# Kernel optimization log

Measured on AMD Instinct MI355X. Metric: run time of the kernel, lower is better.

Reference implementation:

```python
import math
import jax, jax.numpy as jnp
import numpy as np

B, L, D, H = 4, 512, 256, 8
DH = D // H
BUCKETS = 11  # rel_pos_buckets; padding_idx = BUCKETS


def setup_inputs() -> dict:
    key = jax.random.key(0)
    ks = jax.random.split(key, 12)
    s = 0.02
    rel_table = jax.random.normal(ks[10], (BUCKETS + 1, D), dtype=jnp.float32) * s
    rel_table = rel_table.at[BUCKETS].set(0.0)  # padding_idx row is zero
    return {
        "inputs": jax.random.normal(ks[0], (B, L, D), dtype=jnp.float32),
        "mask": jax.random.randint(ks[1], (B, L, L), 0, 2) > 0,
        "distances": jax.random.randint(ks[2], (B, L, L), 0, BUCKETS + 1),
        "Wq": jax.random.normal(ks[3], (D, D), dtype=jnp.float32) * s,
        "bq": jnp.zeros((D,), jnp.float32),
        "Wk": jax.random.normal(ks[4], (D, D), dtype=jnp.float32) * s,
        "bk": jnp.zeros((D,), jnp.float32),
        "Wv": jax.random.normal(ks[5], (D, D), dtype=jnp.float32) * s,
        "bv": jnp.zeros((D,), jnp.float32),
        "Wo": jax.random.normal(ks[6], (D, D), dtype=jnp.float32) * s,
        "bo": jnp.zeros((D,), jnp.float32),
        "rel_table": rel_table,
        "u": jax.random.normal(ks[7], (D,), dtype=jnp.float32) * s,
        "v": jax.random.normal(ks[8], (D,), dtype=jnp.float32) * s,
    }


def reference(inputs, mask, distances, Wq, bq, Wk, bk, Wv, bv, Wo, bo, rel_table, u, v):
    def shape(x):  # (B, L, D) -> (B, H, L, DH)
        return x.reshape(B, L, H, DH).transpose(0, 2, 1, 3)

    q = shape(inputs @ Wq + bq) / math.sqrt(DH)
    k = shape(inputs @ Wk + bk)
    val = shape(inputs @ Wv + bv)

    # content term: (q + u) k^T
    a_c = jnp.einsum("bhqd,bhkd->bhqk", q + u.reshape(1, H, 1, DH), k)

    # relative-position term: embedding gather (padding row already zero, mask anyway)
    valid = (distances != BUCKETS)[..., None].astype(rel_table.dtype)
    rel = (rel_table[distances] * valid).reshape(B, L, L, H, DH)  # (B, Lq, Lk, H, DH)
    b_d = jnp.einsum("bhqd,bqkhd->bhqk", q + v.reshape(1, H, 1, DH), rel)

    scores = jnp.where(mask[:, None, :, :], jnp.float32(-1e18), a_c + b_d)
    attn = jax.nn.softmax(scores, axis=-1)  # (B, H, Lq, Lk)

    ctx = jnp.einsum("bhqk,bhkd->bhqd", attn, val)
    ctx = ctx.transpose(0, 2, 1, 3).reshape(B, L, D)
    output = ctx @ Wo + bo
    return output, attn
```

## Files before the change

kernel.cpp:

```cpp
#include <hip/hip_runtime.h>
#include <math.h>

#define BB 4
#define LL 512
#define DD 256
#define HH 8
#define DHH 32
#define NB 12

__global__ __launch_bounds__(256) void qkv_kernel(const float* __restrict__ x,
    const float* __restrict__ Wq, const float* __restrict__ bq,
    const float* __restrict__ Wk, const float* __restrict__ bk,
    const float* __restrict__ Wv, const float* __restrict__ bv,
    const float* __restrict__ uvec, const float* __restrict__ vvec,
    float* __restrict__ Qu, float* __restrict__ Qv,
    float* __restrict__ KT, float* __restrict__ V) {
    __shared__ float xs[8][DD];
    const int mat = blockIdx.x >> 8;
    const int r0 = (blockIdx.x & 255) * 8;
    const int t = threadIdx.x;
    const int cg = t & 63, rg = t >> 6;
    const int c0 = cg * 4;
    {
        const float4* xg = (const float4*)(x + r0 * DD);
        float4* xsv = (float4*)&xs[0][0];
        xsv[t] = xg[t];
        xsv[t + 256] = xg[t + 256];
    }
    __syncthreads();
    const float* W    = (mat == 0) ? Wq : (mat == 1) ? Wk : Wv;
    const float* bias = (mat == 0) ? bq : (mat == 1) ? bk : bv;
    float acc[2][4];
#pragma unroll
    for (int r = 0; r < 2; ++r)
#pragma unroll
        for (int c = 0; c < 4; ++c) acc[r][c] = bias[c0 + c];
    for (int i0 = 0; i0 < DD; i0 += 4) {
        float4 wv4[4], xv4[2];
#pragma unroll
        for (int j = 0; j < 4; ++j) wv4[j] = *(const float4*)&W[(i0 + j) * DD + c0];
#pragma unroll
        for (int r = 0; r < 2; ++r) xv4[r] = *(const float4*)&xs[rg * 2 + r][i0];
        const float* wf = (const float*)wv4;
        const float* xf = (const float*)xv4;
#pragma unroll
        for (int r = 0; r < 2; ++r)
#pragma unroll
            for (int j = 0; j < 4; ++j)
#pragma unroll
                for (int c = 0; c < 4; ++c)
                    acc[r][c] = fmaf(xf[r * 4 + j], wf[j * 4 + c], acc[r][c]);
    }
    if (mat == 0) {
        const float s = 0.17677669529663687f;
        const float4 u4 = *(const float4*)&uvec[c0];
        const float4 v4 = *(const float4*)&vvec[c0];
#pragma unroll
        for (int r = 0; r < 2; ++r) {
            const int row = r0 + rg * 2 + r;
            float4 q = make_float4(acc[r][0] * s, acc[r][1] * s, acc[r][2] * s, acc[r][3] * s);
            *(float4*)&Qu[row * DD + c0] = make_float4(q.x + u4.x, q.y + u4.y, q.z + u4.z, q.w + u4.w);
            *(float4*)&Qv[row * DD + c0] = make_float4(q.x + v4.x, q.y + v4.y, q.z + v4.z, q.w + v4.w);
        }
    } else if (mat == 1) {
        const int b = r0 >> 9;
        const int kb = (r0 & 511) + rg * 2;
#pragma unroll
        for (int c = 0; c < 4; ++c) {
            const int col = c0 + c;
            const int h = col >> 5, dd = col & 31;
            float* p = KT + ((long)((b * HH + h) * DHH + dd)) * LL + kb;
            p[0] = acc[0][c];
            p[1] = acc[1][c];
        }
    } else {
#pragma unroll
        for (int r = 0; r < 2; ++r)
            *(float4*)&V[(r0 + rg * 2 + r) * DD + c0] =
                make_float4(acc[r][0], acc[r][1], acc[r][2], acc[r][3]);
    }
}

__global__ __launch_bounds__(512, 4) void scores_ctx_kernel(const float* __restrict__ Qu,
    const float* __restrict__ Qv, const float* __restrict__ KT,
    const float* __restrict__ rel_table, const int* __restrict__ mask,
    const int* __restrict__ dist, const float* __restrict__ V,
    float* __restrict__ attn, float* __restrict__ ctx) {
    __shared__ float Qs[16][DHH];
    __shared__ float Ps[16][NB];
    __shared__ float ss[16 * 512];
    const int blk = blockIdx.x;
    const int h = blk & 7;
    const int rest = blk >> 3;
    const int qt16 = rest & 31;
    const int b = rest >> 5;
    const int q0 = qt16 * 16;
    const int t = threadIdx.x;
    const int w = t >> 6, l = t & 63;

    float* Qv8  = ss;
    float* rels = ss + 512;

    {
        const int r = t >> 5, c = t & 31;
        Qs[r][c]          = Qu[(b * LL + q0 + r) * DD + h * DHH + c];
        Qv8[r * DHH + c]  = Qv[(b * LL + q0 + r) * DD + h * DHH + c];
    }
    if (t < NB * DHH) {
        rels[(t >> 5) * 33 + (t & 31)] = rel_table[(t >> 5) * DD + h * DHH + (t & 31)];
    }
    __syncthreads();
    if (t < 16 * NB) {
        const int bk = t >> 4, r = t & 15;
        float a = 0.f;
#pragma unroll
        for (int d = 0; d < DHH; ++d) a = fmaf(Qv8[r * DHH + d], rels[bk * 33 + d], a);
        Ps[r][bk] = a;
    }
    __syncthreads();

    const int r0 = 2 * w;
    const long kbase = (long)(b * HH + h) * DHH * LL;
    float e0[2][4], e1[2][4];
    float sum0 = 0.f, sum1 = 0.f;
#pragma unroll
    for (int s = 0; s < 2; ++s) {
        const int k0 = 4 * l + 256 * s;
        const int4 dx0 = *(const int4*)&dist[(b * LL + q0 + r0) * LL + k0];
        const int4 dx1 = *(const int4*)&dist[(b * LL + q0 + r0 + 1) * LL + k0];
        const int4 mx0 = *(const int4*)&mask[(b * LL + q0 + r0) * LL + k0];
        const int4 mx1 = *(const int4*)&mask[(b * LL + q0 + r0 + 1) * LL + k0];
        float s0[4], s1[4];
        s0[0] = Ps[r0][dx0.x]; s0[1] = Ps[r0][dx0.y]; s0[2] = Ps[r0][dx0.z]; s0[3] = Ps[r0][dx0.w];
        s1[0] = Ps[r0 + 1][dx1.x]; s1[1] = Ps[r0 + 1][dx1.y]; s1[2] = Ps[r0 + 1][dx1.z]; s1[3] = Ps[r0 + 1][dx1.w];
#pragma unroll
        for (int d8 = 0; d8 < DHH; d8 += 8) {
            float4 kv[8];
#pragma unroll
            for (int j = 0; j < 8; ++j)
                kv[j] = *(const float4*)&KT[kbase + (long)(d8 + j) * LL + k0];
            const float4 q0a = *(const float4*)&Qs[r0][d8];
            const float4 q0b = *(const float4*)&Qs[r0][d8 + 4];
            const float4 q1a = *(const float4*)&Qs[r0 + 1][d8];
            const float4 q1b = *(const float4*)&Qs[r0 + 1][d8 + 4];
            const float* qa0 = (const float*)&q0a;
            const float* qb0 = (const float*)&q0b;
            const float* qa1 = (const float*)&q1a;
            const float* qb1 = (const float*)&q1b;
#pragma unroll
            for (int j = 0; j < 4; ++j) {
                s0[0] = fmaf(qa0[j], kv[j].x, s0[0]);
                s0[1] = fmaf(qa0[j], kv[j].y, s0[1]);
                s0[2] = fmaf(qa0[j], kv[j].z, s0[2]);
                s0[3] = fmaf(qa0[j], kv[j].w, s0[3]);
                s1[0] = fmaf(qa1[j], kv[j].x, s1[0]);
                s1[1] = fmaf(qa1[j], kv[j].y, s1[1]);
                s1[2] = fmaf(qa1[j], kv[j].z, s1[2]);
                s1[3] = fmaf(qa1[j], kv[j].w, s1[3]);
            }
#pragma unroll
            for (int j = 0; j < 4; ++j) {
                s0[0] = fmaf(qb0[j], kv[j + 4].x, s0[0]);
                s0[1] = fmaf(qb0[j], kv[j + 4].y, s0[1]);
                s0[2] = fmaf(qb0[j], kv[j + 4].z, s0[2]);
                s0[3] = fmaf(qb0[j], kv[j + 4].w, s0[3]);
                s1[0] = fmaf(qb1[j], kv[j + 4].x, s1[0]);
                s1[1] = fmaf(qb1[j], kv[j + 4].y, s1[1]);
                s1[2] = fmaf(qb1[j], kv[j + 4].z, s1[2]);
                s1[3] = fmaf(qb1[j], kv[j + 4].w, s1[3]);
            }
        }
        e0[s][0] = mx0.x ? 0.f : __expf(s0[0]);
        e0[s][1] = mx0.y ? 0.f : __expf(s0[1]);
        e0[s][2] = mx0.z ? 0.f : __expf(s0[2]);
        e0[s][3] = mx0.w ? 0.f : __expf(s0[3]);
        e1[s][0] = mx1.x ? 0.f : __expf(s1[0]);
        e1[s][1] = mx1.y ? 0.f : __expf(s1[1]);
        e1[s][2] = mx1.z ? 0.f : __expf(s1[2]);
        e1[s][3] = mx1.w ? 0.f : __expf(s1[3]);
        sum0 += (e0[s][0] + e0[s][1]) + (e0[s][2] + e0[s][3]);
        sum1 += (e1[s][0] + e1[s][1]) + (e1[s][2] + e1[s][3]);
    }
    for (int off = 32; off > 0; off >>= 1) {
        sum0 += __shfl_xor(sum0, off);
        sum1 += __shfl_xor(sum1, off);
    }
    const float inv0 = 1.0f / sum0, inv1 = 1.0f / sum1;
    float* a0 = attn + ((long)(b * HH + h) * LL + q0 + r0) * LL;
    float* a1 = a0 + LL;
#pragma unroll
    for (int s = 0; s < 2; ++s) {
        const int k0 = 4 * l + 256 * s;
        const int ch = k0 >> 7;
        const int oct = (k0 & 127) >> 3;
        const int h4 = k0 & 4;
        const float4 o0 = make_float4(e0[s][0] * inv0, e0[s][1] * inv0, e0[s][2] * inv0, e0[s][3] * inv0);
        const float4 o1 = make_float4(e1[s][0] * inv1, e1[s][1] * inv1, e1[s][2] * inv1, e1[s][3] * inv1);
        *(float4*)&a0[k0] = o0;
        *(float4*)&a1[k0] = o1;
        *(float4*)&ss[r0 * 512 + ch * 128 + (((oct ^ (r0 >> 2)) << 3) | h4)] = o0;
        *(float4*)&ss[(r0 + 1) * 512 + ch * 128 + (((oct ^ ((r0 + 1) >> 2)) << 3) | h4)] = o1;
    }

    const int qt = t & 3;
    const int dt = (t >> 2) & 7;
    const int kg = t >> 5;
    const float* vbase = V + (long)b * LL * DD + h * DHH + dt * 4;
    float acc[4][4];
#pragma unroll
    for (int i = 0; i < 4; ++i)
#pragma unroll
        for (int jd = 0; jd < 4; ++jd) acc[i][jd] = 0.f;
    __syncthreads();
#pragma unroll 1
    for (int c = 0; c < 4; ++c) {
#pragma unroll
        for (int ki = 0; ki < 2; ++ki) {
            float4 sv[4];
#pragma unroll
            for (int i = 0; i < 4; ++i)
                sv[i] = *(const float4*)&ss[(qt * 4 + i) * 512 + c * 128 + (((kg ^ qt) << 3) | (ki << 2))];
#pragma unroll
            for (int j = 0; j < 4; ++j) {
                const int k = c * 128 + (kg << 3) + (ki << 2) + j;
                const float4 vf = *(const float4*)&vbase[k * DD];
                const float w0 = ((const float*)&sv[0])[j];
                const float w1 = ((const float*)&sv[1])[j];
                const float w2 = ((const float*)&sv[2])[j];
                const float w3 = ((const float*)&sv[3])[j];
                acc[0][0] = fmaf(w0, vf.x, acc[0][0]); acc[0][1] = fmaf(w0, vf.y, acc[0][1]);
                acc[0][2] = fmaf(w0, vf.z, acc[0][2]); acc[0][3] = fmaf(w0, vf.w, acc[0][3]);
                acc[1][0] = fmaf(w1, vf.x, acc[1][0]); acc[1][1] = fmaf(w1, vf.y, acc[1][1]);
                acc[1][2] = fmaf(w1, vf.z, acc[1][2]); acc[1][3] = fmaf(w1, vf.w, acc[1][3]);
                acc[2][0] = fmaf(w2, vf.x, acc[2][0]); acc[2][1] = fmaf(w2, vf.y, acc[2][1]);
                acc[2][2] = fmaf(w2, vf.z, acc[2][2]); acc[2][3] = fmaf(w2, vf.w, acc[2][3]);
                acc[3][0] = fmaf(w3, vf.x, acc[3][0]); acc[3][1] = fmaf(w3, vf.y, acc[3][1]);
                acc[3][2] = fmaf(w3, vf.z, acc[3][2]); acc[3][3] = fmaf(w3, vf.w, acc[3][3]);
            }
        }
    }
    __syncthreads();
#pragma unroll
    for (int i = 0; i < 4; ++i)
        *(float4*)&ss[kg * 512 + (qt * 4 + i) * 32 + dt * 4] =
            make_float4(acc[i][0], acc[i][1], acc[i][2], acc[i][3]);
    __syncthreads();
    {
        const int qr = t >> 5, dr = t & 31;
        float r = 0.f;
#pragma unroll
        for (int kg2 = 0; kg2 < 16; ++kg2) r += ss[kg2 * 512 + qr * 32 + dr];
        ctx[(b * LL + q0 + qr) * DD + h * DHH + dr] = r;
    }
}

__global__ __launch_bounds__(256) void outproj_kernel(const float* __restrict__ ctx,
    const float* __restrict__ Wo, const float* __restrict__ bo,
    float* __restrict__ out) {
    __shared__ float xs[4][DD];
    const int r0 = blockIdx.x * 4;
    const int t = threadIdx.x;
    const int rg = t >> 6;
    const int c0 = (t & 63) * 4;
    ((float4*)&xs[0][0])[t] = ((const float4*)(ctx + r0 * DD))[t];
    __syncthreads();
    float4 acc = *(const float4*)&bo[c0];
    for (int i0 = 0; i0 < DD; i0 += 8) {
        float4 wv[8];
#pragma unroll
        for (int j = 0; j < 8; ++j) wv[j] = *(const float4*)&Wo[(i0 + j) * DD + c0];
        const float4 x0 = *(const float4*)&xs[rg][i0];
        const float4 x1 = *(const float4*)&xs[rg][i0 + 4];
        const float* xf0 = (const float*)&x0;
        const float* xf1 = (const float*)&x1;
#pragma unroll
        for (int j = 0; j < 4; ++j) {
            acc.x = fmaf(xf0[j], wv[j].x, acc.x);
            acc.y = fmaf(xf0[j], wv[j].y, acc.y);
            acc.z = fmaf(xf0[j], wv[j].z, acc.z);
            acc.w = fmaf(xf0[j], wv[j].w, acc.w);
        }
#pragma unroll
        for (int j = 0; j < 4; ++j) {
            acc.x = fmaf(xf1[j], wv[j + 4].x, acc.x);
            acc.y = fmaf(xf1[j], wv[j + 4].y, acc.y);
            acc.z = fmaf(xf1[j], wv[j + 4].z, acc.z);
            acc.w = fmaf(xf1[j], wv[j + 4].w, acc.w);
        }
    }
    *(float4*)&out[(r0 + rg) * DD + c0] = acc;
}

extern "C" void kernel_launch(void* const* d_in, const int* in_sizes, int n_in,
                              void* d_out, int out_size, void* d_ws, size_t ws_size,
                              hipStream_t stream) {
    const float* x    = (const float*)d_in[0];
    const int* mk     = (const int*)d_in[1];
    const int* dist   = (const int*)d_in[2];
    const float* Wq = (const float*)d_in[3];
    const float* bq = (const float*)d_in[4];
    const float* Wk = (const float*)d_in[5];
    const float* bk = (const float*)d_in[6];
    const float* Wv = (const float*)d_in[7];
    const float* bv = (const float*)d_in[8];
    const float* Wo = (const float*)d_in[9];
    const float* bo = (const float*)d_in[10];
    const float* rel_table = (const float*)d_in[11];
    const float* uvec = (const float*)d_in[12];
    const float* vvec = (const float*)d_in[13];

    float* out  = (float*)d_out;
    float* attn = out + BB * LL * DD;

    float* Qu = (float*)d_ws;
    float* Qv = Qu + BB * LL * DD;
    float* KT = Qv + BB * LL * DD;
    float* V  = KT + BB * LL * DD;
    float* C  = V + BB * LL * DD;

    qkv_kernel<<<3 * 256, 256, 0, stream>>>(x, Wq, bq, Wk, bk, Wv, bv, uvec, vvec,
                                            Qu, Qv, KT, V);
    scores_ctx_kernel<<<BB * (LL / 16) * HH, 512, 0, stream>>>(Qu, Qv, KT, rel_table,
                                                               mk, dist, V, attn, C);
    outproj_kernel<<<BB * LL / 4, 256, 0, stream>>>(C, Wo, bo, out);
}
```

Measured before the change: 167.7 us.

## Enlarge row tiles in projection GEMMs and split score work across key halves

```diff
diff --git a/kernel.cpp b/kernel.cpp
--- a/kernel.cpp
+++ b/kernel.cpp
@@ -8,75 +8,77 @@
 #define DHH 32
 #define NB 12
 
-__global__ __launch_bounds__(256) void qkv_kernel(const float* __restrict__ x,
+__global__ __launch_bounds__(256, 4) void qkv_kernel(const float* __restrict__ x,
     const float* __restrict__ Wq, const float* __restrict__ bq,
     const float* __restrict__ Wk, const float* __restrict__ bk,
     const float* __restrict__ Wv, const float* __restrict__ bv,
     const float* __restrict__ uvec, const float* __restrict__ vvec,
     float* __restrict__ Qu, float* __restrict__ Qv,
     float* __restrict__ KT, float* __restrict__ V) {
-    __shared__ float xs[8][DD];
-    const int mat = blockIdx.x >> 8;
-    const int r0 = (blockIdx.x & 255) * 8;
+    __shared__ float xs[32][DD];
+    const int mat = blockIdx.x >> 6;
+    const int r0 = (blockIdx.x & 63) * 32;
     const int t = threadIdx.x;
     const int cg = t & 63, rg = t >> 6;
     const int c0 = cg * 4;
     {
         const float4* xg = (const float4*)(x + r0 * DD);
         float4* xsv = (float4*)&xs[0][0];
-        xsv[t] = xg[t];
-        xsv[t + 256] = xg[t + 256];
+#pragma unroll
+        for (int j = 0; j < 8; ++j) xsv[t + 256 * j] = xg[t + 256 * j];
     }
     __syncthreads();
     const float* W    = (mat == 0) ? Wq : (mat == 1) ? Wk : Wv;
     const float* bias = (mat == 0) ? bq : (mat == 1) ? bk : bv;
-    float acc[2][4];
-#pragma unroll
-    for (int r = 0; r < 2; ++r)
+    float acc[8][4];
+#pragma unroll
+    for (int r = 0; r < 8; ++r)
 #pragma unroll
         for (int c = 0; c < 4; ++c) acc[r][c] = bias[c0 + c];
     for (int i0 = 0; i0 < DD; i0 += 4) {
-        float4 wv4[4], xv4[2];
+        float4 wv4[4];
 #pragma unroll
         for (int j = 0; j < 4; ++j) wv4[j] = *(const float4*)&W[(i0 + j) * DD + c0];
-#pragma unroll
-        for (int r = 0; r < 2; ++r) xv4[r] = *(const float4*)&xs[rg * 2 + r][i0];
+        float4 xv[8];
+#pragma unroll
+        for (int r = 0; r < 8; ++r) xv[r] = *(const float4*)&xs[rg * 8 + r][i0];
         const float* wf = (const float*)wv4;
-        const float* xf = (const float*)xv4;
-#pragma unroll
-        for (int r = 0; r < 2; ++r)
+#pragma unroll
+        for (int r = 0; r < 8; ++r) {
+            const float* xf = (const float*)&xv[r];
 #pragma unroll
             for (int j = 0; j < 4; ++j)
 #pragma unroll
                 for (int c = 0; c < 4; ++c)
-                    acc[r][c] = fmaf(xf[r * 4 + j], wf[j * 4 + c], acc[r][c]);
+                    acc[r][c] = fmaf(xf[j], wf[j * 4 + c], acc[r][c]);
+        }
     }
     if (mat == 0) {
         const float s = 0.17677669529663687f;
         const float4 u4 = *(const float4*)&uvec[c0];
         const float4 v4 = *(const float4*)&vvec[c0];
 #pragma unroll
-        for (int r = 0; r < 2; ++r) {
-            const int row = r0 + rg * 2 + r;
+        for (int r = 0; r < 8; ++r) {
+            const int row = r0 + rg * 8 + r;
             float4 q = make_float4(acc[r][0] * s, acc[r][1] * s, acc[r][2] * s, acc[r][3] * s);
             *(float4*)&Qu[row * DD + c0] = make_float4(q.x + u4.x, q.y + u4.y, q.z + u4.z, q.w + u4.w);
             *(float4*)&Qv[row * DD + c0] = make_float4(q.x + v4.x, q.y + v4.y, q.z + v4.z, q.w + v4.w);
         }
     } else if (mat == 1) {
         const int b = r0 >> 9;
-        const int kb = (r0 & 511) + rg * 2;
+        const int kb = (r0 & 511) + rg * 8;
 #pragma unroll
         for (int c = 0; c < 4; ++c) {
             const int col = c0 + c;
             const int h = col >> 5, dd = col & 31;
             float* p = KT + ((long)((b * HH + h) * DHH + dd)) * LL + kb;
-            p[0] = acc[0][c];
-            p[1] = acc[1][c];
+            *(float4*)&p[0] = make_float4(acc[0][c], acc[1][c], acc[2][c], acc[3][c]);
+            *(float4*)&p[4] = make_float4(acc[4][c], acc[5][c], acc[6][c], acc[7][c]);
         }
     } else {
 #pragma unroll
-        for (int r = 0; r < 2; ++r)
-            *(float4*)&V[(r0 + rg * 2 + r) * DD + c0] =
+        for (int r = 0; r < 8; ++r)
+            *(float4*)&V[(r0 + rg * 8 + r) * DD + c0] =
                 make_float4(acc[r][0], acc[r][1], acc[r][2], acc[r][3]);
     }
 }
@@ -88,6 +90,7 @@
     float* __restrict__ attn, float* __restrict__ ctx) {
     __shared__ float Qs[16][DHH];
     __shared__ float Ps[16][NB];
+    __shared__ float psum[2][16];
     __shared__ float ss[16 * 512];
     const int blk = blockIdx.x;
     const int h = blk & 7;
@@ -119,87 +122,116 @@
     }
     __syncthreads();
 
-    const int r0 = 2 * w;
+    const int rw = w & 3, sw = w >> 2;
+    const int r0 = 4 * rw;
+    const int k0 = 4 * l + 256 * sw;
     const long kbase = (long)(b * HH + h) * DHH * LL;
-    float e0[2][4], e1[2][4];
-    float sum0 = 0.f, sum1 = 0.f;
-#pragma unroll
-    for (int s = 0; s < 2; ++s) {
-        const int k0 = 4 * l + 256 * s;
+    float s0[4], s1[4], s2[4], s3[4];
+    {
         const int4 dx0 = *(const int4*)&dist[(b * LL + q0 + r0) * LL + k0];
         const int4 dx1 = *(const int4*)&dist[(b * LL + q0 + r0 + 1) * LL + k0];
+        const int4 dx2 = *(const int4*)&dist[(b * LL + q0 + r0 + 2) * LL + k0];
+        const int4 dx3 = *(const int4*)&dist[(b * LL + q0 + r0 + 3) * LL + k0];
+        s0[0] = Ps[r0][dx0.x];     s0[1] = Ps[r0][dx0.y];     s0[2] = Ps[r0][dx0.z];     s0[3] = Ps[r0][dx0.w];
+        s1[0] = Ps[r0 + 1][dx1.x]; s1[1] = Ps[r0 + 1][dx1.y]; s1[2] = Ps[r0 + 1][dx1.z]; s1[3] = Ps[r0 + 1][dx1.w];
+        s2[0] = Ps[r0 + 2][dx2.x]; s2[1] = Ps[r0 + 2][dx2.y]; s2[2] = Ps[r0 + 2][dx2.z]; s2[3] = Ps[r0 + 2][dx2.w];
+        s3[0] = Ps[r0 + 3][dx3.x]; s3[1] = Ps[r0 + 3][dx3.y]; s3[2] = Ps[r0 + 3][dx3.z]; s3[3] = Ps[r0 + 3][dx3.w];
+    }
+#pragma unroll
+    for (int d8 = 0; d8 < DHH; d8 += 8) {
+        float4 kv[8];
+#pragma unroll
+        for (int j = 0; j < 8; ++j)
+            kv[j] = *(const float4*)&KT[kbase + (long)(d8 + j) * LL + k0];
+        const float4 q0a = *(const float4*)&Qs[r0][d8];
+        const float4 q0b = *(const float4*)&Qs[r0][d8 + 4];
+        const float4 q1a = *(const float4*)&Qs[r0 + 1][d8];
+        const float4 q1b = *(const float4*)&Qs[r0 + 1][d8 + 4];
+        const float4 q2a = *(const float4*)&Qs[r0 + 2][d8];
+        const float4 q2b = *(const float4*)&Qs[r0 + 2][d8 + 4];
+        const float4 q3a = *(const float4*)&Qs[r0 + 3][d8];
+        const float4 q3b = *(const float4*)&Qs[r0 + 3][d8 + 4];
+        const float* qa0 = (const float*)&q0a; const float* qb0 = (const float*)&q0b;
+        const float* qa1 = (const float*)&q1a; const float* qb1 = (const float*)&q1b;
+        const float* qa2 = (const float*)&q2a; const float* qb2 = (const float*)&q2b;
+        const float* qa3 = (const float*)&q3a; const float* qb3 = (const float*)&q3b;
+#pragma unroll
+        for (int j = 0; j < 4; ++j) {
+            s0[0] = fmaf(qa0[j], kv[j].x, s0[0]); s0[1] = fmaf(qa0[j], kv[j].y, s0[1]);
+            s0[2] = fmaf(qa0[j], kv[j].z, s0[2]); s0[3] = fmaf(qa0[j], kv[j].w, s0[3]);
+            s1[0] = fmaf(qa1[j], kv[j].x, s1[0]); s1[1] = fmaf(qa1[j], kv[j].y, s1[1]);
+            s1[2] = fmaf(qa1[j], kv[j].z, s1[2]); s1[3] = fmaf(qa1[j], kv[j].w, s1[3]);
+            s2[0] = fmaf(qa2[j], kv[j].x, s2[0]); s2[1] = fmaf(qa2[j], kv[j].y, s2[1]);
+            s2[2] = fmaf(qa2[j], kv[j].z, s2[2]); s2[3] = fmaf(qa2[j], kv[j].w, s2[3]);
+            s3[0] = fmaf(qa3[j], kv[j].x, s3[0]); s3[1] = fmaf(qa3[j], kv[j].y, s3[1]);
+            s3[2] = fmaf(qa3[j], kv[j].z, s3[2]); s3[3] = fmaf(qa3[j], kv[j].w, s3[3]);
+        }
+#pragma unroll
+        for (int j = 0; j < 4; ++j) {
+            s0[0] = fmaf(qb0[j], kv[j + 4].x, s0[0]); s0[1] = fmaf(qb0[j], kv[j + 4].y, s0[1]);
+            s0[2] = fmaf(qb0[j], kv[j + 4].z, s0[2]); s0[3] = fmaf(qb0[j], kv[j + 4].w, s0[3]);
+            s1[0] = fmaf(qb1[j], kv[j + 4].x, s1[0]); s1[1] = fmaf(qb1[j], kv[j + 4].y, s1[1]);
+            s1[2] = fmaf(qb1[j], kv[j + 4].z, s1[2]); s1[3] = fmaf(qb1[j], kv[j + 4].w, s1[3]);
+            s2[0] = fmaf(qb2[j], kv[j + 4].x, s2[0]); s2[1] = fmaf(qb2[j], kv[j + 4].y, s2[1]);
+            s2[2] = fmaf(qb2[j], kv[j + 4].z, s2[2]); s2[3] = fmaf(qb2[j], kv[j + 4].w, s2[3]);
+            s3[0] = fmaf(qb3[j], kv[j + 4].x, s3[0]); s3[1] = fmaf(qb3[j], kv[j + 4].y, s3[1]);
+            s3[2] = fmaf(qb3[j], kv[j + 4].z, s3[2]); s3[3] = fmaf(qb3[j], kv[j + 4].w, s3[3]);
+        }
+    }
+    float e0[4], e1[4], e2[4], e3[4];
+    {
         const int4 mx0 = *(const int4*)&mask[(b * LL + q0 + r0) * LL + k0];
         const int4 mx1 = *(const int4*)&mask[(b * LL + q0 + r0 + 1) * LL + k0];
-        float s0[4], s1[4];
-        s0[0] = Ps[r0][dx0.x]; s0[1] = Ps[r0][dx0.y]; s0[2] = Ps[r0][dx0.z]; s0[3] = Ps[r0][dx0.w];
-        s1[0] = Ps[r0 + 1][dx1.x]; s1[1] = Ps[r0 + 1][dx1.y]; s1[2] = Ps[r0 + 1][dx1.z]; s1[3] = Ps[r0 + 1][dx1.w];
-#pragma unroll
-        for (int d8 = 0; d8 < DHH; d8 += 8) {
-            float4 kv[8];
-#pragma unroll
-            for (int j = 0; j < 8; ++j)
-                kv[j] = *(const float4*)&KT[kbase + (long)(d8 + j) * LL + k0];
-            const float4 q0a = *(const float4*)&Qs[r0][d8];
-            const float4 q0b = *(const float4*)&Qs[r0][d8 + 4];
-            const float4 q1a = *(const float4*)&Qs[r0 + 1][d8];
-            const float4 q1b = *(const float4*)&Qs[r0 + 1][d8 + 4];
-            const float* qa0 = (const float*)&q0a;
-            const float* qb0 = (const float*)&q0b;
-            const float* qa1 = (const float*)&q1a;
-            const float* qb1 = (const float*)&q1b;
-#pragma unroll
-            for (int j = 0; j < 4; ++j) {
-                s0[0] = fmaf(qa0[j], kv[j].x, s0[0]);
-                s0[1] = fmaf(qa0[j], kv[j].y, s0[1]);
-                s0[2] = fmaf(qa0[j], kv[j].z, s0[2]);
-                s0[3] = fmaf(qa0[j], kv[j].w, s0[3]);
-                s1[0] = fmaf(qa1[j], kv[j].x, s1[0]);
-                s1[1] = fmaf(qa1[j], kv[j].y, s1[1]);
-                s1[2] = fmaf(qa1[j], kv[j].z, s1[2]);
-                s1[3] = fmaf(qa1[j], kv[j].w, s1[3]);
-            }
-#pragma unroll
-            for (int j = 0; j < 4; ++j) {
-                s0[0] = fmaf(qb0[j], kv[j + 4].x, s0[0]);
-                s0[1] = fmaf(qb0[j], kv[j + 4].y, s0[1]);
-                s0[2] = fmaf(qb0[j], kv[j + 4].z, s0[2]);
-                s0[3] = fmaf(qb0[j], kv[j + 4].w, s0[3]);
-                s1[0] = fmaf(qb1[j], kv[j + 4].x, s1[0]);
-                s1[1] = fmaf(qb1[j], kv[j + 4].y, s1[1]);
-                s1[2] = fmaf(qb1[j], kv[j + 4].z, s1[2]);
-                s1[3] = fmaf(qb1[j], kv[j + 4].w, s1[3]);
-            }
-        }
-        e0[s][0] = mx0.x ? 0.f : __expf(s0[0]);
-        e0[s][1] = mx0.y ? 0.f : __expf(s0[1]);
-        e0[s][2] = mx0.z ? 0.f : __expf(s0[2]);
-        e0[s][3] = mx0.w ? 0.f : __expf(s0[3]);
-        e1[s][0] = mx1.x ? 0.f : __expf(s1[0]);
-        e1[s][1] = mx1.y ? 0.f : __expf(s1[1]);
-        e1[s][2] = mx1.z ? 0.f : __expf(s1[2]);
-        e1[s][3] = mx1.w ? 0.f : __expf(s1[3]);
-        sum0 += (e0[s][0] + e0[s][1]) + (e0[s][2] + e0[s][3]);
-        sum1 += (e1[s][0] + e1[s][1]) + (e1[s][2] + e1[s][3]);
-    }
+        const int4 mx2 = *(const int4*)&mask[(b * LL + q0 + r0 + 2) * LL + k0];
+        const int4 mx3 = *(const int4*)&mask[(b * LL + q0 + r0 + 3) * LL + k0];
+        e0[0] = mx0.x ? 0.f : __expf(s0[0]); e0[1] = mx0.y ? 0.f : __expf(s0[1]);
+        e0[2] = mx0.z ? 0.f : __expf(s0[2]); e0[3] = mx0.w ? 0.f : __expf(s0[3]);
+        e1[0] = mx1.x ? 0.f : __expf(s1[0]); e1[1] = mx1.y ? 0.f : __expf(s1[1]);
+        e1[2] = mx1.z ? 0.f : __expf(s1[2]); e1[3] = mx1.w ? 0.f : __expf(s1[3]);
+        e2[0] = mx2.x ? 0.f : __expf(s2[0]); e2[1] = mx2.y ? 0.f : __expf(s2[1]);
+        e2[2] = mx2.z ? 0.f : __expf(s2[2]); e2[3] = mx2.w ? 0.f : __expf(s2[3]);
+        e3[0] = mx3.x ? 0.f : __expf(s3[0]); e3[1] = mx3.y ? 0.f : __expf(s3[1]);
+        e3[2] = mx3.z ? 0.f : __expf(s3[2]); e3[3] = mx3.w ? 0.f : __expf(s3[3]);
+    }
+    float sm0 = (e0[0] + e0[1]) + (e0[2] + e0[3]);
+    float sm1 = (e1[0] + e1[1]) + (e1[2] + e1[3]);
+    float sm2 = (e2[0] + e2[1]) + (e2[2] + e2[3]);
+    float sm3 = (e3[0] + e3[1]) + (e3[2] + e3[3]);
     for (int off = 32; off > 0; off >>= 1) {
-        sum0 += __shfl_xor(sum0, off);
-        sum1 += __shfl_xor(sum1, off);
-    }
-    const float inv0 = 1.0f / sum0, inv1 = 1.0f / sum1;
-    float* a0 = attn + ((long)(b * HH + h) * LL + q0 + r0) * LL;
-    float* a1 = a0 + LL;
-#pragma unroll
-    for (int s = 0; s < 2; ++s) {
-        const int k0 = 4 * l + 256 * s;
+        sm0 += __shfl_xor(sm0, off);
+        sm1 += __shfl_xor(sm1, off);
+        sm2 += __shfl_xor(sm2, off);
+        sm3 += __shfl_xor(sm3, off);
+    }
+    if (l == 0) {
+        psum[sw][r0]     = sm0;
+        psum[sw][r0 + 1] = sm1;
+        psum[sw][r0 + 2] = sm2;
+        psum[sw][r0 + 3] = sm3;
+    }
+    __syncthreads();
+    const float inv0 = 1.0f / (psum[0][r0]     + psum[1][r0]);
+    const float inv1 = 1.0f / (psum[0][r0 + 1] + psum[1][r0 + 1]);
+    const float inv2 = 1.0f / (psum[0][r0 + 2] + psum[1][r0 + 2]);
+    const float inv3 = 1.0f / (psum[0][r0 + 3] + psum[1][r0 + 3]);
+    {
+        float* a0 = attn + ((long)(b * HH + h) * LL + q0 + r0) * LL + k0;
         const int ch = k0 >> 7;
         const int oct = (k0 & 127) >> 3;
         const int h4 = k0 & 4;
-        const float4 o0 = make_float4(e0[s][0] * inv0, e0[s][1] * inv0, e0[s][2] * inv0, e0[s][3] * inv0);
-        const float4 o1 = make_float4(e1[s][0] * inv1, e1[s][1] * inv1, e1[s][2] * inv1, e1[s][3] * inv1);
-        *(float4*)&a0[k0] = o0;
-        *(float4*)&a1[k0] = o1;
-        *(float4*)&ss[r0 * 512 + ch * 128 + (((oct ^ (r0 >> 2)) << 3) | h4)] = o0;
-        *(float4*)&ss[(r0 + 1) * 512 + ch * 128 + (((oct ^ ((r0 + 1) >> 2)) << 3) | h4)] = o1;
+        const int sbase = ch * 128 + (((oct ^ rw) << 3) | h4);
+        const float4 o0 = make_float4(e0[0] * inv0, e0[1] * inv0, e0[2] * inv0, e0[3] * inv0);
+        const float4 o1 = make_float4(e1[0] * inv1, e1[1] * inv1, e1[2] * inv1, e1[3] * inv1);
+        const float4 o2 = make_float4(e2[0] * inv2, e2[1] * inv2, e2[2] * inv2, e2[3] * inv2);
+        const float4 o3 = make_float4(e3[0] * inv3, e3[1] * inv3, e3[2] * inv3, e3[3] * inv3);
+        *(float4*)&a0[0]      = o0;
+        *(float4*)&a0[LL]     = o1;
+        *(float4*)&a0[2 * LL] = o2;
+        *(float4*)&a0[3 * LL] = o3;
+        *(float4*)&ss[(r0)     * 512 + sbase] = o0;
+        *(float4*)&ss[(r0 + 1) * 512 + sbase] = o1;
+        *(float4*)&ss[(r0 + 2) * 512 + sbase] = o2;
+        *(float4*)&ss[(r0 + 3) * 512 + sbase] = o3;
     }
 
     const int qt = t & 3;
@@ -254,41 +286,51 @@
     }
 }
 
-__global__ __launch_bounds__(256) void outproj_kernel(const float* __restrict__ ctx,
+__global__ __launch_bounds__(256, 4) void outproj_kernel(const float* __restrict__ ctx,
     const float* __restrict__ Wo, const float* __restrict__ bo,
     float* __restrict__ out) {
-    __shared__ float xs[4][DD];
-    const int r0 = blockIdx.x * 4;
+    __shared__ float xs[32][DD];
+    const int r0 = blockIdx.x * 32;
     const int t = threadIdx.x;
-    const int rg = t >> 6;
-    const int c0 = (t & 63) * 4;
-    ((float4*)&xs[0][0])[t] = ((const float4*)(ctx + r0 * DD))[t];
-    __syncthreads();
-    float4 acc = *(const float4*)&bo[c0];
-    for (int i0 = 0; i0 < DD; i0 += 8) {
-        float4 wv[8];
-#pragma unroll
-        for (int j = 0; j < 8; ++j) wv[j] = *(const float4*)&Wo[(i0 + j) * DD + c0];
-        const float4 x0 = *(const float4*)&xs[rg][i0];
-        const float4 x1 = *(const float4*)&xs[rg][i0 + 4];
-        const float* xf0 = (const float*)&x0;
-        const float* xf1 = (const float*)&x1;
-#pragma unroll
-        for (int j = 0; j < 4; ++j) {
-            acc.x = fmaf(xf0[j], wv[j].x, acc.x);
-            acc.y = fmaf(xf0[j], wv[j].y, acc.y);
-            acc.z = fmaf(xf0[j], wv[j].z, acc.z);
-            acc.w = fmaf(xf0[j], wv[j].w, acc.w);
-        }
-#pragma unroll
-        for (int j = 0; j < 4; ++j) {
-            acc.x = fmaf(xf1[j], wv[j + 4].x, acc.x);
-            acc.y = fmaf(xf1[j], wv[j + 4].y, acc.y);
-            acc.z = fmaf(xf1[j], wv[j + 4].z, acc.z);
-            acc.w = fmaf(xf1[j], wv[j + 4].w, acc.w);
-        }
-    }
-    *(float4*)&out[(r0 + rg) * DD + c0] = acc;
+    const int cg = t & 63, rg = t >> 6;
+    const int c0 = cg * 4;
+    {
+        const float4* xg = (const float4*)(ctx + r0 * DD);
+        float4* xsv = (float4*)&xs[0][0];
+#pragma unroll
+        for (int j = 0; j < 8; ++j) xsv[t + 256 * j] = xg[t + 256 * j];
+    }
+    __syncthreads();
+    float acc[8][4];
+    {
+        const float4 b4 = *(const float4*)&bo[c0];
+#pragma unroll
+        for (int r = 0; r < 8; ++r) {
+            acc[r][0] = b4.x; acc[r][1] = b4.y; acc[r][2] = b4.z; acc[r][3] = b4.w;
+        }
+    }
+    for (int i0 = 0; i0 < DD; i0 += 4) {
+        float4 wv4[4];
+#pragma unroll
+        for (int j = 0; j < 4; ++j) wv4[j] = *(const float4*)&Wo[(i0 + j) * DD + c0];
+        float4 xv[8];
+#pragma unroll
+        for (int r = 0; r < 8; ++r) xv[r] = *(const float4*)&xs[rg * 8 + r][i0];
+        const float* wf = (const float*)wv4;
+#pragma unroll
+        for (int r = 0; r < 8; ++r) {
+            const float* xf = (const float*)&xv[r];
+#pragma unroll
+            for (int j = 0; j < 4; ++j)
+#pragma unroll
+                for (int c = 0; c < 4; ++c)
+                    acc[r][c] = fmaf(xf[j], wf[j * 4 + c], acc[r][c]);
+        }
+    }
+#pragma unroll
+    for (int r = 0; r < 8; ++r)
+        *(float4*)&out[(r0 + rg * 8 + r) * DD + c0] =
+            make_float4(acc[r][0], acc[r][1], acc[r][2], acc[r][3]);
 }
 
 extern "C" void kernel_launch(void* const* d_in, const int* in_sizes, int n_in,
@@ -318,9 +360,9 @@
     float* V  = KT + BB * LL * DD;
     float* C  = V + BB * LL * DD;
 
-    qkv_kernel<<<3 * 256, 256, 0, stream>>>(x, Wq, bq, Wk, bk, Wv, bv, uvec, vvec,
-                                            Qu, Qv, KT, V);
+    qkv_kernel<<<3 * 64, 256, 0, stream>>>(x, Wq, bq, Wk, bk, Wv, bv, uvec, vvec,
+                                           Qu, Qv, KT, V);
     scores_ctx_kernel<<<BB * (LL / 16) * HH, 512, 0, stream>>>(Qu, Qv, KT, rel_table,
                                                                mk, dist, V, attn, C);
-    outproj_kernel<<<BB * LL / 4, 256, 0, stream>>>(C, Wo, bo, out);
+    outproj_kernel<<<BB * LL / 32, 256, 0, stream>>>(C, Wo, bo, out);
 }
```

After: 188.7 us. 12.5% more time.

## Double query tile to 32 rows per block to increase K/V reuse

Applied to the files above, without the earlier changes.

```diff
diff --git a/kernel.cpp b/kernel.cpp
--- a/kernel.cpp
+++ b/kernel.cpp
@@ -86,32 +86,35 @@
     const float* __restrict__ rel_table, const int* __restrict__ mask,
     const int* __restrict__ dist, const float* __restrict__ V,
     float* __restrict__ attn, float* __restrict__ ctx) {
-    __shared__ float Qs[16][DHH];
-    __shared__ float Ps[16][NB];
-    __shared__ float ss[16 * 512];
+    __shared__ float Qs[32][DHH];
+    __shared__ float Ps[32][NB];
+    __shared__ float psum[2][32];
+    __shared__ float ss[32 * 512];
     const int blk = blockIdx.x;
     const int h = blk & 7;
     const int rest = blk >> 3;
-    const int qt16 = rest & 31;
-    const int b = rest >> 5;
-    const int q0 = qt16 * 16;
+    const int qt32 = rest & 15;
+    const int b = rest >> 4;
+    const int q0 = qt32 * 32;
     const int t = threadIdx.x;
     const int w = t >> 6, l = t & 63;
 
     float* Qv8  = ss;
-    float* rels = ss + 512;
+    float* rels = ss + 1024;
 
     {
-        const int r = t >> 5, c = t & 31;
-        Qs[r][c]          = Qu[(b * LL + q0 + r) * DD + h * DHH + c];
-        Qv8[r * DHH + c]  = Qv[(b * LL + q0 + r) * DD + h * DHH + c];
+        const int r = t >> 4, c2 = (t & 15) * 2;
+        const float2 qu2 = *(const float2*)&Qu[(b * LL + q0 + r) * DD + h * DHH + c2];
+        const float2 qv2 = *(const float2*)&Qv[(b * LL + q0 + r) * DD + h * DHH + c2];
+        Qs[r][c2]     = qu2.x;  Qs[r][c2 + 1]     = qu2.y;
+        Qv8[r * DHH + c2] = qv2.x;  Qv8[r * DHH + c2 + 1] = qv2.y;
     }
     if (t < NB * DHH) {
         rels[(t >> 5) * 33 + (t & 31)] = rel_table[(t >> 5) * DD + h * DHH + (t & 31)];
     }
     __syncthreads();
-    if (t < 16 * NB) {
-        const int bk = t >> 4, r = t & 15;
+    if (t < 32 * NB) {
+        const int bk = t >> 5, r = t & 31;
         float a = 0.f;
 #pragma unroll
         for (int d = 0; d < DHH; ++d) a = fmaf(Qv8[r * DHH + d], rels[bk * 33 + d], a);
@@ -119,92 +122,76 @@
     }
     __syncthreads();
 
-    const int r0 = 2 * w;
+    const int rw = w & 3, sw = w >> 2;
+    const int r0 = 8 * rw;
+    const int k0 = 4 * l + 256 * sw;
     const long kbase = (long)(b * HH + h) * DHH * LL;
-    float e0[2][4], e1[2][4];
-    float sum0 = 0.f, sum1 = 0.f;
-#pragma unroll
-    for (int s = 0; s < 2; ++s) {
-        const int k0 = 4 * l + 256 * s;
-        const int4 dx0 = *(const int4*)&dist[(b * LL + q0 + r0) * LL + k0];
-        const int4 dx1 = *(const int4*)&dist[(b * LL + q0 + r0 + 1) * LL + k0];
-        const int4 mx0 = *(const int4*)&mask[(b * LL + q0 + r0) * LL + k0];
-        const int4 mx1 = *(const int4*)&mask[(b * LL + q0 + r0 + 1) * LL + k0];
-        float s0[4], s1[4];
-        s0[0] = Ps[r0][dx0.x]; s0[1] = Ps[r0][dx0.y]; s0[2] = Ps[r0][dx0.z]; s0[3] = Ps[r0][dx0.w];
-        s1[0] = Ps[r0 + 1][dx1.x]; s1[1] = Ps[r0 + 1][dx1.y]; s1[2] = Ps[r0 + 1][dx1.z]; s1[3] = Ps[r0 + 1][dx1.w];
-#pragma unroll
-        for (int d8 = 0; d8 < DHH; d8 += 8) {
-            float4 kv[8];
-#pragma unroll
-            for (int j = 0; j < 8; ++j)
-                kv[j] = *(const float4*)&KT[kbase + (long)(d8 + j) * LL + k0];
-            const float4 q0a = *(const float4*)&Qs[r0][d8];
-            const float4 q0b = *(const float4*)&Qs[r0][d8 + 4];
-            const float4 q1a = *(const float4*)&Qs[r0 + 1][d8];
-            const float4 q1b = *(const float4*)&Qs[r0 + 1][d8 + 4];
-            const float* qa0 = (const float*)&q0a;
-            const float* qb0 = (const float*)&q0b;
-            const float* qa1 = (const float*)&q1a;
-            const float* qb1 = (const float*)&q1b;
+    float sc[8][4];
+#pragma unroll
+    for (int r = 0; r < 8; ++r) {
+        const int4 dx = *(const int4*)&dist[(b * LL + q0 + r0 + r) * LL + k0];
+        sc[r][0] = Ps[r0 + r][dx.x];  sc[r][1] = Ps[r0 + r][dx.y];
+        sc[r][2] = Ps[r0 + r][dx.z];  sc[r][3] = Ps[r0 + r][dx.w];
+    }
+#pragma unroll 1
+    for (int d8 = 0; d8 < DHH; d8 += 8) {
+        float4 kv[8];
+#pragma unroll
+        for (int j = 0; j < 8; ++j)
+            kv[j] = *(const float4*)&KT[kbase + (long)(d8 + j) * LL + k0];
+#pragma unroll
+        for (int r = 0; r < 8; ++r) {
+            const float4 qa4 = *(const float4*)&Qs[r0 + r][d8];
+            const float4 qb4 = *(const float4*)&Qs[r0 + r][d8 + 4];
+            const float* qa = (const float*)&qa4;
+            const float* qb = (const float*)&qb4;
 #pragma unroll
             for (int j = 0; j < 4; ++j) {
-                s0[0] = fmaf(qa0[j], kv[j].x, s0[0]);
-                s0[1] = fmaf(qa0[j], kv[j].y, s0[1]);
-                s0[2] = fmaf(qa0[j], kv[j].z, s0[2]);
-                s0[3] = fmaf(qa0[j], kv[j].w, s0[3]);
-                s1[0] = fmaf(qa1[j], kv[j].x, s1[0]);
-                s1[1] = fmaf(qa1[j], kv[j].y, s1[1]);
-                s1[2] = fmaf(qa1[j], kv[j].z, s1[2]);
-                s1[3] = fmaf(qa1[j], kv[j].w, s1[3]);
+                sc[r][0] = fmaf(qa[j], kv[j].x, sc[r][0]);
+                sc[r][1] = fmaf(qa[j], kv[j].y, sc[r][1]);
+                sc[r][2] = fmaf(qa[j], kv[j].z, sc[r][2]);
+                sc[r][3] = fmaf(qa[j], kv[j].w, sc[r][3]);
             }
 #pragma unroll
             for (int j = 0; j < 4; ++j) {
-                s0[0] = fmaf(qb0[j], kv[j + 4].x, s0[0]);
-                s0[1] = fmaf(qb0[j], kv[j + 4].y, s0[1]);
-                s0[2] = fmaf(qb0[j], kv[j + 4].z, s0[2]);
-                s0[3] = fmaf(qb0[j], kv[j + 4].w, s0[3]);
-                s1[0] = fmaf(qb1[j], kv[j + 4].x, s1[0]);
-                s1[1] = fmaf(qb1[j], kv[j + 4].y, s1[1]);
-                s1[2] = fmaf(qb1[j], kv[j + 4].z, s1[2]);
-                s1[3] = fmaf(qb1[j], kv[j + 4].w, s1[3]);
+                sc[r][0] = fmaf(qb[j], kv[j + 4].x, sc[r][0]);
+                sc[r][1] = fmaf(qb[j], kv[j + 4].y, sc[r][1]);
+                sc[r][2] = fmaf(qb[j], kv[j + 4].z, sc[r][2]);
+                sc[r][3] = fmaf(qb[j], kv[j + 4].w, sc[r][3]);
             }
         }
-        e0[s][0] = mx0.x ? 0.f : __expf(s0[0]);
-        e0[s][1] = mx0.y ? 0.f : __expf(s0[1]);
-        e0[s][2] = mx0.z ? 0.f : __expf(s0[2]);
-        e0[s][3] = mx0.w ? 0.f : __expf(s0[3]);
-        e1[s][0] = mx1.x ? 0.f : __expf(s1[0]);
-        e1[s][1] = mx1.y ? 0.f : __expf(s1[1]);
-        e1[s][2] = mx1.z ? 0.f : __expf(s1[2]);
-        e1[s][3] = mx1.w ? 0.f : __expf(s1[3]);
-        sum0 += (e0[s][0] + e0[s][1]) + (e0[s][2] + e0[s][3]);
-        sum1 += (e1[s][0] + e1[s][1]) + (e1[s][2] + e1[s][3]);
-    }
-    for (int off = 32; off > 0; off >>= 1) {
-        sum0 += __shfl_xor(sum0, off);
-        sum1 += __shfl_xor(sum1, off);
-    }
-    const float inv0 = 1.0f / sum0, inv1 = 1.0f / sum1;
-    float* a0 = attn + ((long)(b * HH + h) * LL + q0 + r0) * LL;
-    float* a1 = a0 + LL;
-#pragma unroll
-    for (int s = 0; s < 2; ++s) {
-        const int k0 = 4 * l + 256 * s;
+    }
+    float ev[8][4];
+#pragma unroll
+    for (int r = 0; r < 8; ++r) {
+        const int4 mx = *(const int4*)&mask[(b * LL + q0 + r0 + r) * LL + k0];
+        ev[r][0] = mx.x ? 0.f : __expf(sc[r][0]);
+        ev[r][1] = mx.y ? 0.f : __expf(sc[r][1]);
+        ev[r][2] = mx.z ? 0.f : __expf(sc[r][2]);
+        ev[r][3] = mx.w ? 0.f : __expf(sc[r][3]);
+        float sm = (ev[r][0] + ev[r][1]) + (ev[r][2] + ev[r][3]);
+        for (int off = 32; off > 0; off >>= 1) sm += __shfl_xor(sm, off);
+        if (l == 0) psum[sw][r0 + r] = sm;
+    }
+    __syncthreads();
+    {
         const int ch = k0 >> 7;
         const int oct = (k0 & 127) >> 3;
         const int h4 = k0 & 4;
-        const float4 o0 = make_float4(e0[s][0] * inv0, e0[s][1] * inv0, e0[s][2] * inv0, e0[s][3] * inv0);
-        const float4 o1 = make_float4(e1[s][0] * inv1, e1[s][1] * inv1, e1[s][2] * inv1, e1[s][3] * inv1);
-        *(float4*)&a0[k0] = o0;
-        *(float4*)&a1[k0] = o1;
-        *(float4*)&ss[r0 * 512 + ch * 128 + (((oct ^ (r0 >> 2)) << 3) | h4)] = o0;
-        *(float4*)&ss[(r0 + 1) * 512 + ch * 128 + (((oct ^ ((r0 + 1) >> 2)) << 3) | h4)] = o1;
-    }
-
-    const int qt = t & 3;
-    const int dt = (t >> 2) & 7;
-    const int kg = t >> 5;
+#pragma unroll
+        for (int r = 0; r < 8; ++r) {
+            const int q = r0 + r;
+            const float inv = 1.0f / (psum[0][q] + psum[1][q]);
+            const float4 o = make_float4(ev[r][0] * inv, ev[r][1] * inv,
+                                         ev[r][2] * inv, ev[r][3] * inv);
+            *(float4*)&attn[((long)(b * HH + h) * LL + q0 + q) * LL + k0] = o;
+            *(float4*)&ss[q * 512 + ch * 128 + (((oct ^ (q >> 2)) << 3) | h4)] = o;
+        }
+    }
+
+    const int qt = t & 7;
+    const int dt = (t >> 3) & 7;
+    const int kg = t >> 6;
     const float* vbase = V + (long)b * LL * DD + h * DHH + dt * 4;
     float acc[4][4];
 #pragma unroll
@@ -215,42 +202,50 @@
 #pragma unroll 1
     for (int c = 0; c < 4; ++c) {
 #pragma unroll
-        for (int ki = 0; ki < 2; ++ki) {
-            float4 sv[4];
-#pragma unroll
-            for (int i = 0; i < 4; ++i)
-                sv[i] = *(const float4*)&ss[(qt * 4 + i) * 512 + c * 128 + (((kg ^ qt) << 3) | (ki << 2))];
-#pragma unroll
-            for (int j = 0; j < 4; ++j) {
-                const int k = c * 128 + (kg << 3) + (ki << 2) + j;
-                const float4 vf = *(const float4*)&vbase[k * DD];
-                const float w0 = ((const float*)&sv[0])[j];
-                const float w1 = ((const float*)&sv[1])[j];
-                const float w2 = ((const float*)&sv[2])[j];
-                const float w3 = ((const float*)&sv[3])[j];
-                acc[0][0] = fmaf(w0, vf.x, acc[0][0]); acc[0][1] = fmaf(w0, vf.y, acc[0][1]);
-                acc[0][2] = fmaf(w0, vf.z, acc[0][2]); acc[0][3] = fmaf(w0, vf.w, acc[0][3]);
-                acc[1][0] = fmaf(w1, vf.x, acc[1][0]); acc[1][1] = fmaf(w1, vf.y, acc[1][1]);
-                acc[1][2] = fmaf(w1, vf.z, acc[1][2]); acc[1][3] = fmaf(w1, vf.w, acc[1][3]);
-                acc[2][0] = fmaf(w2, vf.x, acc[2][0]); acc[2][1] = fmaf(w2, vf.y, acc[2][1]);
-                acc[2][2] = fmaf(w2, vf.z, acc[2][2]); acc[2][3] = fmaf(w2, vf.w, acc[2][3]);
-                acc[3][0] = fmaf(w3, vf.x, acc[3][0]); acc[3][1] = fmaf(w3, vf.y, acc[3][1]);
-                acc[3][2] = fmaf(w3, vf.z, acc[3][2]); acc[3][3] = fmaf(w3, vf.w, acc[3][3]);
+        for (int oo = 0; oo < 2; ++oo) {
+            const int o = kg + 8 * oo;
+#pragma unroll
+            for (int ki = 0; ki < 2; ++ki) {
+                float4 sv[4];
+#pragma unroll
+                for (int i = 0; i < 4; ++i)
+                    sv[i] = *(const float4*)&ss[(qt * 4 + i) * 512 + c * 128 + (((o ^ qt) << 3) | (ki << 2))];
+#pragma unroll
+                for (int j = 0; j < 4; ++j) {
+                    const int k = c * 128 + (o << 3) + (ki << 2) + j;
+                    const float4 vf = *(const float4*)&vbase[k * DD];
+                    const float w0 = ((const float*)&sv[0])[j];
+                    const float w1 = ((const float*)&sv[1])[j];
+                    const float w2 = ((const float*)&sv[2])[j];
+                    const float w3 = ((const float*)&sv[3])[j];
+                    acc[0][0] = fmaf(w0, vf.x, acc[0][0]); acc[0][1] = fmaf(w0, vf.y, acc[0][1]);
+                    acc[0][2] = fmaf(w0, vf.z, acc[0][2]); acc[0][3] = fmaf(w0, vf.w, acc[0][3]);
+                    acc[1][0] = fmaf(w1, vf.x, acc[1][0]); acc[1][1] = fmaf(w1, vf.y, acc[1][1]);
+                    acc[1][2] = fmaf(w1, vf.z, acc[1][2]); acc[1][3] = fmaf(w1, vf.w, acc[1][3]);
+                    acc[2][0] = fmaf(w2, vf.x, acc[2][0]); acc[2][1] = fmaf(w2, vf.y, acc[2][1]);
+                    acc[2][2] = fmaf(w2, vf.z, acc[2][2]); acc[2][3] = fmaf(w2, vf.w, acc[2][3]);
+                    acc[3][0] = fmaf(w3, vf.x, acc[3][0]); acc[3][1] = fmaf(w3, vf.y, acc[3][1]);
+                    acc[3][2] = fmaf(w3, vf.z, acc[3][2]); acc[3][3] = fmaf(w3, vf.w, acc[3][3]);
+                }
             }
         }
     }
     __syncthreads();
 #pragma unroll
     for (int i = 0; i < 4; ++i)
-        *(float4*)&ss[kg * 512 + (qt * 4 + i) * 32 + dt * 4] =
+        *(float4*)&ss[kg * 1024 + (qt * 4 + i) * 32 + dt * 4] =
             make_float4(acc[i][0], acc[i][1], acc[i][2], acc[i][3]);
     __syncthreads();
     {
-        const int qr = t >> 5, dr = t & 31;
-        float r = 0.f;
-#pragma unroll
-        for (int kg2 = 0; kg2 < 16; ++kg2) r += ss[kg2 * 512 + qr * 32 + dr];
-        ctx[(b * LL + q0 + qr) * DD + h * DHH + dr] = r;
+        const int qr = t >> 4;
+        const int d2 = (t & 15) * 2;
+        float v0 = 0.f, v1 = 0.f;
+#pragma unroll
+        for (int g = 0; g < 8; ++g) {
+            const float2 p = *(const float2*)&ss[g * 1024 + qr * 32 + d2];
+            v0 += p.x; v1 += p.y;
+        }
+        *(float2*)&ctx[(b * LL + q0 + qr) * DD + h * DHH + d2] = make_float2(v0, v1);
     }
 }
 
@@ -320,7 +315,7 @@
 
     qkv_kernel<<<3 * 256, 256, 0, stream>>>(x, Wq, bq, Wk, bk, Wv, bv, uvec, vvec,
                                             Qu, Qv, KT, V);
-    scores_ctx_kernel<<<BB * (LL / 16) * HH, 512, 0, stream>>>(Qu, Qv, KT, rel_table,
+    scores_ctx_kernel<<<BB * (LL / 32) * HH, 512, 0, stream>>>(Qu, Qv, KT, rel_table,
                                                                mk, dist, V, attn, C);
     outproj_kernel<<<BB * LL / 4, 256, 0, stream>>>(C, Wo, bo, out);
 }
```

Result: no change. 165.8 us (-1.2%).
